# Kernel tuning notes

Hardware: AMD Instinct MI355X
Metric: run time of the kernel (lower is better)

The kernel has to match this reference:

```python
import jax, jax.numpy as jnp
import numpy as np

DIM = 1024
HEADS = 16
DIM_HEAD = 64
INNER = HEADS * DIM_HEAD  # 1024
FEAT = 1024  # cfg.different_learnable_tokens=False -> feature_dim = dim
EPS = 1e-5
SCALE = 1.0 / np.sqrt(DIM_HEAD)


def setup_inputs() -> dict:
    key = jax.random.key(0)
    ks = jax.random.split(key, 10)
    b, n = 2, 2048
    x = jax.random.normal(ks[0], (b, n, DIM), jnp.float32)
    y = jax.random.normal(ks[1], (b, n, FEAT), jnp.float32)
    # learned parameters
    ln_g = jnp.ones((DIM,), jnp.float32)
    ln_b = jnp.zeros((DIM,), jnp.float32)
    w_qkv = jax.random.normal(ks[2], (DIM, 3 * INNER), jnp.float32) * (DIM ** -0.5)
    w_av = jax.random.normal(ks[3], (FEAT, INNER), jnp.float32) * (FEAT ** -0.5)
    w_out = jax.random.normal(ks[4], (INNER, DIM), jnp.float32) * (INNER ** -0.5)
    b_out = jnp.zeros((DIM,), jnp.float32)
    w_yout = jax.random.normal(ks[5], (INNER, FEAT), jnp.float32) * (INNER ** -0.5)
    b_yout = jnp.zeros((FEAT,), jnp.float32)
    return {"x": x, "y": y, "ln_g": ln_g, "ln_b": ln_b, "w_qkv": w_qkv,
            "w_av": w_av, "w_out": w_out, "b_out": b_out,
            "w_yout": w_yout, "b_yout": b_yout}


def _split_heads(t):  # [b,n,(h d)] -> [b,h,n,d]
    b, n, _ = t.shape
    return t.reshape(b, n, HEADS, DIM_HEAD).transpose(0, 2, 1, 3)


def _merge_heads(t):  # [b,h,n,d] -> [b,n,(h d)]
    b, h, n, d = t.shape
    return t.transpose(0, 2, 1, 3).reshape(b, n, h * d)


def reference(x, y, ln_g, ln_b, w_qkv, w_av, w_out, b_out, w_yout, b_yout):
    # LayerNorm
    mu = jnp.mean(x, axis=-1, keepdims=True)
    var = jnp.mean(jnp.square(x - mu), axis=-1, keepdims=True)
    xn = (x - mu) * jax.lax.rsqrt(var + EPS) * ln_g + ln_b

    qkv = xn @ w_qkv  # [b,n,3*inner]
    q, k, v = jnp.split(qkv, 3, axis=-1)
    av = y @ w_av  # [b,n,inner]
    q, k, v, av = map(_split_heads, (q, k, v, av))  # [b,h,n,d]

    # shared QK softmax, applied to both V and another_v
    scores = jnp.einsum('bhnd,bhmd->bhnm', q, k) * SCALE
    attn = jax.nn.softmax(scores, axis=-1)
    x_ctx = jnp.einsum('bhnm,bhmd->bhnd', attn, v)
    y_ctx = jnp.einsum('bhnm,bhmd->bhnd', attn, av)

    x_out = _merge_heads(x_ctx) @ w_out + b_out
    y_out = _merge_heads(y_ctx) @ w_yout + b_yout
    return (x_out, y_out)
```

## Files before the change

### kernel.cpp

```cpp
#include <hip/hip_runtime.h>

typedef _Float16 half8 __attribute__((ext_vector_type(8)));
typedef _Float16 half4v __attribute__((ext_vector_type(4)));
typedef float f32x4 __attribute__((ext_vector_type(4)));
typedef unsigned int u32;

#define SEQ 2048
#define NTOK 4096
#define DM 1024
#define QKS 2048
#define LN_EPS 1e-5f
#define LOG2E_SCALE 0.18033688f

typedef const __attribute__((address_space(1))) u32* gas_ptr;
typedef __attribute__((address_space(3))) u32* las_ptr;
__device__ __forceinline__ void gld_lds16(const void* g, void* l) {
  __builtin_amdgcn_global_load_lds((gas_ptr)g, (las_ptr)l, 16, 0, 0);
}

#define BARRIER() do { __builtin_amdgcn_s_barrier(); __builtin_amdgcn_sched_barrier(0); } while (0)
#define VMW(N) do { asm volatile("s_waitcnt vmcnt(" #N ")" ::: "memory"); __builtin_amdgcn_sched_barrier(0); } while (0)
#define LGW() do { asm volatile("s_waitcnt lgkmcnt(0)" ::: "memory"); __builtin_amdgcn_sched_barrier(0); } while (0)

__global__ __launch_bounds__(256) void prep_kernel(
    const float* __restrict__ x, const float* __restrict__ g, const float* __restrict__ bta,
    const float* __restrict__ y,
    const float* __restrict__ w_qkv, const float* __restrict__ w_av,
    const float* __restrict__ w_out, const float* __restrict__ w_yout,
    _Float16* __restrict__ xn, _Float16* __restrict__ yh,
    _Float16* __restrict__ wqkvT, _Float16* __restrict__ wavT,
    _Float16* __restrict__ woutT, _Float16* __restrict__ wyoutT) {
  __shared__ float smem[64 * 65];
  const int bid = blockIdx.x;
  const int t = threadIdx.x;
  if (bid < 4096) {
    const int row = bid;
    const float4 v = ((const float4*)(x + (size_t)row * DM))[t];
    float s = v.x + v.y + v.z + v.w;
#pragma unroll
    for (int m = 1; m < 64; m <<= 1) s += __shfl_xor(s, m, 64);
    float* red = smem;
    const int wid = t >> 6, lane = t & 63;
    if (lane == 0) red[wid] = s;
    __syncthreads();
    const float mu = (red[0] + red[1] + red[2] + red[3]) * (1.0f / DM);
    const float dx = v.x - mu, dy = v.y - mu, dz = v.z - mu, dw = v.w - mu;
    float ss = dx * dx + dy * dy + dz * dz + dw * dw;
#pragma unroll
    for (int m = 1; m < 64; m <<= 1) ss += __shfl_xor(ss, m, 64);
    __syncthreads();
    if (lane == 0) red[wid] = ss;
    __syncthreads();
    const float var = (red[0] + red[1] + red[2] + red[3]) * (1.0f / DM);
    const float rstd = rsqrtf(var + LN_EPS);
    const float4 gg = ((const float4*)g)[t];
    const float4 bb = ((const float4*)bta)[t];
    half4v o;
    o[0] = (_Float16)(dx * rstd * gg.x + bb.x);
    o[1] = (_Float16)(dy * rstd * gg.y + bb.y);
    o[2] = (_Float16)(dz * rstd * gg.z + bb.z);
    o[3] = (_Float16)(dw * rstd * gg.w + bb.w);
    *(half4v*)(xn + (size_t)row * DM + t * 4) = o;
  } else if (bid < 8192) {
    const int row = bid - 4096;
    const float4 v = ((const float4*)(y + (size_t)row * DM))[t];
    half4v o;
    o[0] = (_Float16)v.x; o[1] = (_Float16)v.y;
    o[2] = (_Float16)v.z; o[3] = (_Float16)v.w;
    *(half4v*)(yh + (size_t)row * DM + t * 4) = o;
  } else {
    const int id2 = bid - 8192;
    const float* W; _Float16* WT; int Nc, bx, by;
    if (id2 < 768) { W = w_qkv; WT = wqkvT; Nc = 3072; bx = id2 % 48; by = id2 / 48; }
    else {
      const int id3 = id2 - 768, sel = id3 >> 8;
      Nc = 1024; bx = id3 & 15; by = (id3 >> 4) & 15;
      if (sel == 0) { W = w_av; WT = wavT; }
      else if (sel == 1) { W = w_out; WT = woutT; }
      else { W = w_yout; WT = wyoutT; }
    }
    float (*tile)[65] = (float(*)[65])smem;
    const int n0 = bx * 64, k0 = by * 64;
    const int c = t & 63;
#pragma unroll
    for (int i = 0; i < 16; i++) {
      const int r = (t >> 6) * 16 + i;
      tile[r][c] = W[(size_t)(k0 + r) * Nc + n0 + c];
    }
    __syncthreads();
#pragma unroll
    for (int i = 0; i < 16; i++) {
      const int n = (t >> 6) * 16 + i;
      WT[(size_t)(n0 + n) * 1024 + k0 + c] = (_Float16)tile[c][n];
    }
  }
}

__global__ __launch_bounds__(512, 2) void gemm8p_kernel(
    const _Float16* __restrict__ xn, const _Float16* __restrict__ wqkvT,
    const _Float16* __restrict__ yh, const _Float16* __restrict__ wavT,
    _Float16* __restrict__ qkvm, _Float16* __restrict__ vtb,
    _Float16* __restrict__ avtb) {
  __shared__ _Float16 Ab[2][8192];
  __shared__ _Float16 Bb[2][8192];
  const int swz = ((blockIdx.x & 7) << 5) + (blockIdx.x >> 3);
  const _Float16 *A, *B;
  int m0, n0, isav;
  if (swz < 192) { A = xn; B = wqkvT; m0 = (swz / 12) * 256; n0 = (swz % 12) * 256; isav = 0; }
  else { const int u = swz - 192; A = yh; B = wavT; m0 = (u >> 2) * 256; n0 = (u & 3) * 256; isav = 1; }
  const int t = threadIdx.x;
  const int wid = t >> 6, lane = t & 63, lo = lane & 15, hi = lane >> 4;
  const int wm = wid >> 2, wn = wid & 3;
  const int srow = t >> 2;
  const int sx = ((t & 3) ^ (srow & 3)) << 3;
  const _Float16* gA = A + (size_t)(m0 + srow) * 1024 + sx;
  const _Float16* gB = B + (size_t)(n0 + srow) * 1024 + sx;
  const int rdz = (hi ^ (lo & 3)) << 3;
  const int arow = (wm * 128 + lo) * 32 + rdz;
  const int brow = (wn * 64 + lo) * 32 + rdz;

  f32x4 acc[8][4];
#pragma unroll
  for (int i = 0; i < 8; i++)
#pragma unroll
    for (int j = 0; j < 4; j++) {
      acc[i][j][0] = 0.f; acc[i][j][1] = 0.f; acc[i][j][2] = 0.f; acc[i][j][3] = 0.f;
    }
  half8 af[4], bf[4];

#define STG_A(BUF, HH, KT) gld_lds16(gA + (HH) * 131072 + (KT) * 32, &Ab[BUF][(HH) * 4096 + t * 8])
#define STG_B(BUF, HH, KT) gld_lds16(gB + (HH) * 131072 + (KT) * 32, &Bb[BUF][(HH) * 4096 + t * 8])
#define RDA(BUF, FB)                                                     \
  _Pragma("unroll") for (int f2 = 0; f2 < 4; f2++)                       \
      af[f2] = *(const half8*)&Ab[BUF][arow + ((FB) + f2) * 512]
#define RDB(BUF, G0)                                                     \
  _Pragma("unroll") for (int g2 = 0; g2 < 2; g2++)                       \
      bf[(G0) + g2] = *(const half8*)&Bb[BUF][brow + ((G0) + g2) * 512]
#define MMA(FB, G0)                                                      \
  do {                                                                   \
    __builtin_amdgcn_s_setprio(1);                                       \
    _Pragma("unroll") for (int f2 = 0; f2 < 4; f2++)                     \
        _Pragma("unroll") for (int g2 = 0; g2 < 2; g2++)                 \
            acc[(FB) + f2][(G0) + g2] = __builtin_amdgcn_mfma_f32_16x16x32_f16( \
                af[f2], bf[(G0) + g2], acc[(FB) + f2][(G0) + g2], 0, 0, 0); \
    __builtin_amdgcn_s_setprio(0);                                       \
  } while (0)

  STG_A(0, 0, 0); STG_A(0, 1, 0); STG_B(0, 0, 0); STG_B(0, 1, 0);
  STG_A(1, 0, 1);

  for (int it = 0; it < 16; it++) {
    const int T1 = 2 * it + 1;
    const int N0 = (2 * it + 2) & 31, N1 = (2 * it + 3) & 31;
    VMW(1); BARRIER();
    RDA(0, 0); RDB(0, 0);
    STG_A(1, 1, T1);
    LGW(); MMA(0, 0);
    BARRIER(); RDB(0, 2); STG_B(1, 0, T1); LGW(); MMA(0, 2);
    BARRIER(); RDA(0, 4); STG_B(1, 1, T1); LGW(); MMA(4, 2);
    BARRIER(); STG_A(0, 0, N0); MMA(4, 0);
    VMW(1); BARRIER();
    RDA(1, 0); RDB(1, 0);
    STG_A(0, 1, N0);
    LGW(); MMA(0, 0);
    BARRIER(); RDB(1, 2); STG_B(0, 0, N0); LGW(); MMA(0, 2);
    BARRIER(); RDA(1, 4); STG_B(0, 1, N0); LGW(); MMA(4, 2);
    BARRIER(); STG_A(1, 0, N1); MMA(4, 0);
  }
#undef STG_A
#undef STG_B
#undef RDA
#undef RDB
#undef MMA

#pragma unroll
  for (int f = 0; f < 8; f++)
#pragma unroll
    for (int g = 0; g < 4; g++)
#pragma unroll
      for (int r = 0; r < 4; r++) {
        const int row = m0 + wm * 128 + f * 16 + 4 * hi + r;
        const int col = n0 + wn * 64 + g * 16 + lo;
        const _Float16 v = (_Float16)acc[f][g][r];
        if (!isav && col < 2048) {
          qkvm[(size_t)row * QKS + col] = v;
        } else {
          const int coff = isav ? col : col - 2048;
          _Float16* Ct = isav ? avtb : vtb;
          Ct[(((size_t)((row >> 11) << 4) + (coff >> 6)) * 64 + (coff & 63)) * SEQ +
             (row & (SEQ - 1))] = v;
        }
      }
}

__global__ __launch_bounds__(512, 2) void gemmout8p_kernel(
    const _Float16* __restrict__ xc, const _Float16* __restrict__ woutT,
    float* __restrict__ o0, const float* __restrict__ b0,
    const _Float16* __restrict__ yc, const _Float16* __restrict__ wyoutT,
    float* __restrict__ o1, const float* __restrict__ b1) {
  __shared__ _Float16 Ab[2][8192];
  __shared__ _Float16 Bb[2][8192];
  const int swz = ((blockIdx.x & 7) << 4) + (blockIdx.x >> 3);
  const _Float16 *A, *B;
  float* F; const float* bias;
  int u;
  if (swz < 64) { A = xc; B = woutT; F = o0; bias = b0; u = swz; }
  else { A = yc; B = wyoutT; F = o1; bias = b1; u = swz - 64; }
  const int m0 = (u >> 2) * 256, n0 = (u & 3) * 256;
  const int t = threadIdx.x;
  const int wid = t >> 6, lane = t & 63, lo = lane & 15, hi = lane >> 4;
  const int wm = wid >> 2, wn = wid & 3;
  const int srow = t >> 2;
  const int sx = ((t & 3) ^ (srow & 3)) << 3;
  const _Float16* gA = A + (size_t)(m0 + srow) * 1024 + sx;
  const _Float16* gB = B + (size_t)(n0 + srow) * 1024 + sx;
  const int rdz = (hi ^ (lo & 3)) << 3;
  const int arow = (wm * 128 + lo) * 32 + rdz;
  const int brow = (wn * 64 + lo) * 32 + rdz;

  f32x4 acc[8][4];
#pragma unroll
  for (int i = 0; i < 8; i++)
#pragma unroll
    for (int j = 0; j < 4; j++) {
      acc[i][j][0] = 0.f; acc[i][j][1] = 0.f; acc[i][j][2] = 0.f; acc[i][j][3] = 0.f;
    }
  half8 af[4], bf[4];

#define STG_A(BUF, HH, KT) gld_lds16(gA + (HH) * 131072 + (KT) * 32, &Ab[BUF][(HH) * 4096 + t * 8])
#define STG_B(BUF, HH, KT) gld_lds16(gB + (HH) * 131072 + (KT) * 32, &Bb[BUF][(HH) * 4096 + t * 8])
#define RDA(BUF, FB)                                                     \
  _Pragma("unroll") for (int f2 = 0; f2 < 4; f2++)                       \
      af[f2] = *(const half8*)&Ab[BUF][arow + ((FB) + f2) * 512]
#define RDB(BUF, G0)                                                     \
  _Pragma("unroll") for (int g2 = 0; g2 < 2; g2++)                       \
      bf[(G0) + g2] = *(const half8*)&Bb[BUF][brow + ((G0) + g2) * 512]
#define MMA(FB, G0)                                                      \
  do {                                                                   \
    __builtin_amdgcn_s_setprio(1);                                       \
    _Pragma("unroll") for (int f2 = 0; f2 < 4; f2++)                     \
        _Pragma("unroll") for (int g2 = 0; g2 < 2; g2++)                 \
            acc[(FB) + f2][(G0) + g2] = __builtin_amdgcn_mfma_f32_16x16x32_f16( \
                af[f2], bf[(G0) + g2], acc[(FB) + f2][(G0) + g2], 0, 0, 0); \
    __builtin_amdgcn_s_setprio(0);                                       \
  } while (0)

  STG_A(0, 0, 0); STG_A(0, 1, 0); STG_B(0, 0, 0); STG_B(0, 1, 0);
  STG_A(1, 0, 1);

  for (int it = 0; it < 16; it++) {
    const int T1 = 2 * it + 1;
    const int N0 = (2 * it + 2) & 31, N1 = (2 * it + 3) & 31;
    VMW(1); BARRIER();
    RDA(0, 0); RDB(0, 0);
    STG_A(1, 1, T1);
    LGW(); MMA(0, 0);
    BARRIER(); RDB(0, 2); STG_B(1, 0, T1); LGW(); MMA(0, 2);
    BARRIER(); RDA(0, 4); STG_B(1, 1, T1); LGW(); MMA(4, 2);
    BARRIER(); STG_A(0, 0, N0); MMA(4, 0);
    VMW(1); BARRIER();
    RDA(1, 0); RDB(1, 0);
    STG_A(0, 1, N0);
    LGW(); MMA(0, 0);
    BARRIER(); RDB(1, 2); STG_B(0, 0, N0); LGW(); MMA(0, 2);
    BARRIER(); RDA(1, 4); STG_B(0, 1, N0); LGW(); MMA(4, 2);
    BARRIER(); STG_A(1, 0, N1); MMA(4, 0);
  }
#undef STG_A
#undef STG_B
#undef RDA
#undef RDB
#undef MMA

#pragma unroll
  for (int f = 0; f < 8; f++)
#pragma unroll
    for (int g = 0; g < 4; g++)
#pragma unroll
      for (int r = 0; r < 4; r++) {
        const int row = m0 + wm * 128 + f * 16 + 4 * hi + r;
        const int col = n0 + wn * 64 + g * 16 + lo;
        F[(size_t)row * 1024 + col] = acc[f][g][r] + bias[col];
      }
}

__global__ __launch_bounds__(256, 4) void attn_kernel(
    const _Float16* __restrict__ qkvm,
    const _Float16* __restrict__ vt,
    const _Float16* __restrict__ avt,
    _Float16* __restrict__ xctx, _Float16* __restrict__ yctx) {
  __shared__ _Float16 Kl[2][2048];
  __shared__ _Float16 Vl[2][2048];
  __shared__ _Float16 Al[2][2048];
  __shared__ _Float16 Pl[4][512];

  const int t = threadIdx.x;
  const int wid = t >> 6, lane = t & 63, lo = lane & 15, hi = lane >> 4;
  const int id = blockIdx.x;
  const int bh = ((id & 7) << 2) + ((id >> 3) >> 5);
  const int qt = (id >> 3) & 31;
  const int b = bh >> 4, h = bh & 15;
  const int q0 = qt * 64 + wid * 16;
  const size_t tokbase = (size_t)b * SEQ;
  const _Float16* vbase = vt + (size_t)bh * 64 * SEQ;
  const _Float16* abase = avt + (size_t)bh * 64 * SEQ;
  _Float16* Pw = Pl[wid];
  const int NT = SEQ / 32;
  const int swzP = (lo & 3) ^ ((lo >> 2) & 3);

  half8 qf[2];
#pragma unroll
  for (int kc = 0; kc < 2; kc++)
    qf[kc] = *(const half8*)(qkvm + (tokbase + q0 + lo) * QKS +
                             h * 64 + kc * 32 + hi * 8);

  f32x4 zero;
  zero[0] = 0.f; zero[1] = 0.f; zero[2] = 0.f; zero[3] = 0.f;
  f32x4 accx[4], accy[4];
  float mC = -1.0e30f, lsum = 0.0f;
#pragma unroll
  for (int j = 0; j < 4; j++) { accx[j] = zero; accy[j] = zero; }

  const int kkey = t >> 3, kc7 = t & 7;
  const int vrow = t >> 2, vc3 = t & 3;
  const int kcs = ((kc7 ^ (kkey & 7)) << 3);
  const int vcs = ((vc3 ^ ((vrow & 3) ^ ((vrow >> 2) & 3))) << 3);

#define STAGE(kv0, BSEL)                                                          \
  do {                                                                            \
    gld_lds16(qkvm + (tokbase + (kv0) + kkey) * QKS + DM + h * 64 + kcs,          \
              &Kl[BSEL][(t >> 6) * 512 + (t & 63) * 8]);                          \
    gld_lds16(vbase + (size_t)vrow * SEQ + (kv0) + vcs,                           \
              &Vl[BSEL][(t >> 6) * 512 + (t & 63) * 8]);                          \
    gld_lds16(abase + (size_t)vrow * SEQ + (kv0) + vcs,                           \
              &Al[BSEL][(t >> 6) * 512 + (t & 63) * 8]);                          \
  } while (0)

  STAGE(0, 0);
  int bsel = 0;
  for (int tt = 0; tt < NT; tt++) {
    __syncthreads();
    if (tt + 1 < NT) STAGE((tt + 1) * 32, bsel ^ 1);
    const _Float16* Kb = Kl[bsel];
    const _Float16* Vb = Vl[bsel];
    const _Float16* Ab = Al[bsel];

    f32x4 s[2];
#pragma unroll
    for (int kg = 0; kg < 2; kg++) {
      const int krow = kg * 16 + lo;
      const int kr = krow * 64;
      const half8 ak0 = *(const half8*)(Kb + kr + ((hi ^ (krow & 7)) << 3));
      const half8 ak1 = *(const half8*)(Kb + kr + (((4 | hi) ^ (krow & 7)) << 3));
      f32x4 z = __builtin_amdgcn_mfma_f32_16x16x32_f16(ak0, qf[0], zero, 0, 0, 0);
      s[kg] = __builtin_amdgcn_mfma_f32_16x16x32_f16(ak1, qf[1], z, 0, 0, 0);
    }

    float tm = -3.0e38f;
#pragma unroll
    for (int kg = 0; kg < 2; kg++)
#pragma unroll
      for (int r = 0; r < 4; r++) tm = fmaxf(tm, s[kg][r]);
    tm = fmaxf(tm, __shfl_xor(tm, 16, 64));
    tm = fmaxf(tm, __shfl_xor(tm, 32, 64));
    const float tmC = tm * LOG2E_SCALE;

    if (__any(tmC > mC + 8.0f)) {
      const float mn = fmaxf(mC, tmC);
      const float fcs = exp2f(mC - mn);
      mC = mn;
      lsum *= fcs;
#pragma unroll
      for (int r = 0; r < 4; r++) {
        const float fcb = __shfl(fcs, 4 * hi + r, 64);
#pragma unroll
        for (int ng = 0; ng < 4; ng++) {
          accx[ng][r] *= fcb;
          accy[ng][r] *= fcb;
        }
      }
    }

    {
      float rs = 0.0f;
#pragma unroll
      for (int kg = 0; kg < 2; kg++) {
        half4v pk;
#pragma unroll
        for (int r = 0; r < 4; r++) {
          const float p = exp2f(fmaf(s[kg][r], LOG2E_SCALE, -mC));
          rs += p;
          pk[r] = (_Float16)p;
        }
        *(half4v*)(Pw + lo * 32 +
                   (((kg * 2 + (hi >> 1)) ^ swzP) << 3) + ((hi & 1) << 2)) = pk;
      }
      rs += __shfl_xor(rs, 16, 64);
      rs += __shfl_xor(rs, 32, 64);
      lsum += rs;
    }

    {
      const half8 pa = *(const half8*)(Pw + lo * 32 + ((hi ^ swzP) << 3));
#pragma unroll
      for (int ng = 0; ng < 4; ng++) {
        const int vrow2 = ng * 16 + lo;
        const int vr = vrow2 * 32 + ((hi ^ ((vrow2 & 3) ^ ((vrow2 >> 2) & 3))) << 3);
        const half8 bv = *(const half8*)(Vb + vr);
        const half8 ba = *(const half8*)(Ab + vr);
        accx[ng] = __builtin_amdgcn_mfma_f32_16x16x32_f16(pa, bv, accx[ng], 0, 0, 0);
        accy[ng] = __builtin_amdgcn_mfma_f32_16x16x32_f16(pa, ba, accy[ng], 0, 0, 0);
      }
    }
    bsel ^= 1;
  }
#undef STAGE

  const float inv = 1.0f / lsum;
#pragma unroll
  for (int r = 0; r < 4; r++) {
    const float invb = __shfl(inv, 4 * hi + r, 64);
    const size_t tok = tokbase + q0 + 4 * hi + r;
#pragma unroll
    for (int ng = 0; ng < 4; ng++) {
      const int col = h * 64 + ng * 16 + lo;
      xctx[tok * DM + col] = (_Float16)(accx[ng][r] * invb);
      yctx[tok * DM + col] = (_Float16)(accy[ng][r] * invb);
    }
  }
}

extern "C" void kernel_launch(void* const* d_in, const int* in_sizes, int n_in,
                              void* d_out, int out_size, void* d_ws, size_t ws_size,
                              hipStream_t stream) {
  const float* x      = (const float*)d_in[0];
  const float* y      = (const float*)d_in[1];
  const float* ln_g   = (const float*)d_in[2];
  const float* ln_b   = (const float*)d_in[3];
  const float* w_qkv  = (const float*)d_in[4];
  const float* w_av   = (const float*)d_in[5];
  const float* w_out  = (const float*)d_in[6];
  const float* b_out  = (const float*)d_in[7];
  const float* w_yout = (const float*)d_in[8];
  const float* b_yout = (const float*)d_in[9];
  float* out = (float*)d_out;

  _Float16* ws     = (_Float16*)d_ws;
  _Float16* xn     = ws;
  _Float16* yh     = xn + 4194304;
  _Float16* wqkvT  = yh + 4194304;
  _Float16* wavT   = wqkvT + 3145728;
  _Float16* woutT  = wavT + 1048576;
  _Float16* wyoutT = woutT + 1048576;
  _Float16* qkvm   = wyoutT + 1048576;
  _Float16* vtb    = qkvm + 8388608;
  _Float16* avtb   = vtb + 4194304;
  _Float16* xc     = avtb + 4194304;
  _Float16* yc     = xc + 4194304;

  prep_kernel<<<9728, 256, 0, stream>>>(x, ln_g, ln_b, y, w_qkv, w_av, w_out, w_yout,
                                        xn, yh, wqkvT, wavT, woutT, wyoutT);

  gemm8p_kernel<<<256, 512, 0, stream>>>(xn, wqkvT, yh, wavT, qkvm, vtb, avtb);

  attn_kernel<<<1024, 256, 0, stream>>>(qkvm, vtb, avtb, xc, yc);

  gemmout8p_kernel<<<128, 512, 0, stream>>>(
      xc, woutT, out, b_out,
      yc, wyoutT, out + 4194304, b_yout);
}
```

Baseline: 210.7 us.

## Deepen QKV GEMM K-tile, simplify output GEMM, defer softmax reductions

```diff
diff --git a/kernel.cpp b/kernel.cpp
--- a/kernel.cpp
+++ b/kernel.cpp
@@ -96,13 +96,13 @@
   }
 }
 
-__global__ __launch_bounds__(512, 2) void gemm8p_kernel(
+__global__ __launch_bounds__(512, 1) void gemm8p_kernel(
     const _Float16* __restrict__ xn, const _Float16* __restrict__ wqkvT,
     const _Float16* __restrict__ yh, const _Float16* __restrict__ wavT,
     _Float16* __restrict__ qkvm, _Float16* __restrict__ vtb,
     _Float16* __restrict__ avtb) {
-  __shared__ _Float16 Ab[2][8192];
-  __shared__ _Float16 Bb[2][8192];
+  __shared__ _Float16 Ab[2][16384];
+  __shared__ _Float16 Bb[2][16384];
   const int swz = ((blockIdx.x & 7) << 5) + (blockIdx.x >> 3);
   const _Float16 *A, *B;
   int m0, n0, isav;
@@ -111,13 +111,14 @@
   const int t = threadIdx.x;
   const int wid = t >> 6, lane = t & 63, lo = lane & 15, hi = lane >> 4;
   const int wm = wid >> 2, wn = wid & 3;
-  const int srow = t >> 2;
-  const int sx = ((t & 3) ^ (srow & 3)) << 3;
-  const _Float16* gA = A + (size_t)(m0 + srow) * 1024 + sx;
-  const _Float16* gB = B + (size_t)(n0 + srow) * 1024 + sx;
-  const int rdz = (hi ^ (lo & 3)) << 3;
-  const int arow = (wm * 128 + lo) * 32 + rdz;
-  const int brow = (wn * 64 + lo) * 32 + rdz;
+  const int srow = t >> 3;
+  const int schk = t & 7;
+  const _Float16* gA = A + (size_t)(m0 + srow) * 1024 + ((schk ^ (srow & 7)) << 3);
+  const _Float16* gB = B + (size_t)(n0 + srow) * 1024 + ((schk ^ (srow & 7)) << 3);
+  const int arow = (wm * 128 + lo) * 64;
+  const int brow = (wn * 64 + lo) * 64;
+  const int rz0 = ((hi ^ (lo & 7)) << 3);
+  const int rz1 = (((4 | hi) ^ (lo & 7)) << 3);
 
   f32x4 acc[8][4];
 #pragma unroll
@@ -126,52 +127,58 @@
     for (int j = 0; j < 4; j++) {
       acc[i][j][0] = 0.f; acc[i][j][1] = 0.f; acc[i][j][2] = 0.f; acc[i][j][3] = 0.f;
     }
-  half8 af[4], bf[4];
-
-#define STG_A(BUF, HH, KT) gld_lds16(gA + (HH) * 131072 + (KT) * 32, &Ab[BUF][(HH) * 4096 + t * 8])
-#define STG_B(BUF, HH, KT) gld_lds16(gB + (HH) * 131072 + (KT) * 32, &Bb[BUF][(HH) * 4096 + t * 8])
-#define RDA(BUF, FB)                                                     \
-  _Pragma("unroll") for (int f2 = 0; f2 < 4; f2++)                       \
-      af[f2] = *(const half8*)&Ab[BUF][arow + ((FB) + f2) * 512]
-#define RDB(BUF, G0)                                                     \
-  _Pragma("unroll") for (int g2 = 0; g2 < 2; g2++)                       \
-      bf[(G0) + g2] = *(const half8*)&Bb[BUF][brow + ((G0) + g2) * 512]
-#define MMA(FB, G0)                                                      \
-  do {                                                                   \
-    __builtin_amdgcn_s_setprio(1);                                       \
-    _Pragma("unroll") for (int f2 = 0; f2 < 4; f2++)                     \
-        _Pragma("unroll") for (int g2 = 0; g2 < 2; g2++)                 \
-            acc[(FB) + f2][(G0) + g2] = __builtin_amdgcn_mfma_f32_16x16x32_f16( \
-                af[f2], bf[(G0) + g2], acc[(FB) + f2][(G0) + g2], 0, 0, 0); \
-    __builtin_amdgcn_s_setprio(0);                                       \
+  half8 af[4][2], bf[4][2];
+
+#define STG_A(BUF, P, KT) gld_lds16(gA + (P) * 65536 + (KT) * 64, &Ab[BUF][(P) * 4096 + t * 8])
+#define STG_B(BUF, P, KT) gld_lds16(gB + (P) * 65536 + (KT) * 64, &Bb[BUF][(P) * 4096 + t * 8])
+#define RDA8(BUF, FB)                                                       \
+  _Pragma("unroll") for (int f2 = 0; f2 < 4; f2++) {                        \
+    af[f2][0] = *(const half8*)&Ab[BUF][arow + ((FB) + f2) * 1024 + rz0];   \
+    af[f2][1] = *(const half8*)&Ab[BUF][arow + ((FB) + f2) * 1024 + rz1];   \
+  }
+#define RDB4(BUF, G0)                                                       \
+  _Pragma("unroll") for (int g2 = 0; g2 < 2; g2++) {                        \
+    bf[(G0) + g2][0] = *(const half8*)&Bb[BUF][brow + ((G0) + g2) * 1024 + rz0]; \
+    bf[(G0) + g2][1] = *(const half8*)&Bb[BUF][brow + ((G0) + g2) * 1024 + rz1]; \
+  }
+#define MMA16(FB, G0)                                                       \
+  do {                                                                      \
+    __builtin_amdgcn_s_setprio(1);                                          \
+    _Pragma("unroll") for (int f2 = 0; f2 < 4; f2++)                        \
+      _Pragma("unroll") for (int g2 = 0; g2 < 2; g2++)                      \
+        _Pragma("unroll") for (int ks = 0; ks < 2; ks++)                    \
+          acc[(FB) + f2][(G0) + g2] = __builtin_amdgcn_mfma_f32_16x16x32_f16( \
+              af[f2][ks], bf[(G0) + g2][ks], acc[(FB) + f2][(G0) + g2], 0, 0, 0); \
+    __builtin_amdgcn_s_setprio(0);                                          \
   } while (0)
 
-  STG_A(0, 0, 0); STG_A(0, 1, 0); STG_B(0, 0, 0); STG_B(0, 1, 0);
-  STG_A(1, 0, 1);
-
-  for (int it = 0; it < 16; it++) {
+  STG_A(0, 0, 0); STG_A(0, 1, 0); STG_A(0, 2, 0); STG_A(0, 3, 0);
+  STG_B(0, 0, 0); STG_B(0, 1, 0); STG_B(0, 2, 0); STG_B(0, 3, 0);
+  STG_A(1, 0, 1); STG_A(1, 1, 1);
+
+  for (int it = 0; it < 8; it++) {
     const int T1 = 2 * it + 1;
-    const int N0 = (2 * it + 2) & 31, N1 = (2 * it + 3) & 31;
-    VMW(1); BARRIER();
-    RDA(0, 0); RDB(0, 0);
-    STG_A(1, 1, T1);
-    LGW(); MMA(0, 0);
-    BARRIER(); RDB(0, 2); STG_B(1, 0, T1); LGW(); MMA(0, 2);
-    BARRIER(); RDA(0, 4); STG_B(1, 1, T1); LGW(); MMA(4, 2);
-    BARRIER(); STG_A(0, 0, N0); MMA(4, 0);
-    VMW(1); BARRIER();
-    RDA(1, 0); RDB(1, 0);
-    STG_A(0, 1, N0);
-    LGW(); MMA(0, 0);
-    BARRIER(); RDB(1, 2); STG_B(0, 0, N0); LGW(); MMA(0, 2);
-    BARRIER(); RDA(1, 4); STG_B(0, 1, N0); LGW(); MMA(4, 2);
-    BARRIER(); STG_A(1, 0, N1); MMA(4, 0);
+    const int N0 = (2 * it + 2) & 15, N1 = (2 * it + 3) & 15;
+    VMW(2); BARRIER();
+    RDA8(0, 0); RDB4(0, 0);
+    STG_A(1, 2, T1); STG_A(1, 3, T1);
+    LGW(); MMA16(0, 0);
+    BARRIER(); RDB4(0, 2); STG_B(1, 0, T1); STG_B(1, 1, T1); LGW(); MMA16(0, 2);
+    BARRIER(); RDA8(0, 4); STG_B(1, 2, T1); STG_B(1, 3, T1); LGW(); MMA16(4, 2);
+    BARRIER(); STG_A(0, 0, N0); STG_A(0, 1, N0); MMA16(4, 0);
+    VMW(2); BARRIER();
+    RDA8(1, 0); RDB4(1, 0);
+    STG_A(0, 2, N0); STG_A(0, 3, N0);
+    LGW(); MMA16(0, 0);
+    BARRIER(); RDB4(1, 2); STG_B(0, 0, N0); STG_B(0, 1, N0); LGW(); MMA16(0, 2);
+    BARRIER(); RDA8(1, 4); STG_B(0, 2, N0); STG_B(0, 3, N0); LGW(); MMA16(4, 2);
+    BARRIER(); STG_A(1, 0, N1); STG_A(1, 1, N1); MMA16(4, 0);
   }
 #undef STG_A
 #undef STG_B
-#undef RDA
-#undef RDB
-#undef MMA
+#undef RDA8
+#undef RDB4
+#undef MMA16
 
 #pragma unroll
   for (int f = 0; f < 8; f++)
@@ -193,94 +200,66 @@
       }
 }
 
-__global__ __launch_bounds__(512, 2) void gemmout8p_kernel(
-    const _Float16* __restrict__ xc, const _Float16* __restrict__ woutT,
-    float* __restrict__ o0, const float* __restrict__ b0,
-    const _Float16* __restrict__ yc, const _Float16* __restrict__ wyoutT,
-    float* __restrict__ o1, const float* __restrict__ b1) {
-  __shared__ _Float16 Ab[2][8192];
-  __shared__ _Float16 Bb[2][8192];
-  const int swz = ((blockIdx.x & 7) << 4) + (blockIdx.x >> 3);
-  const _Float16 *A, *B;
-  float* F; const float* bias;
-  int u;
-  if (swz < 64) { A = xc; B = woutT; F = o0; bias = b0; u = swz; }
-  else { A = yc; B = wyoutT; F = o1; bias = b1; u = swz - 64; }
-  const int m0 = (u >> 2) * 256, n0 = (u & 3) * 256;
+__global__ __launch_bounds__(256) void gemmout_kernel(
+    const _Float16* __restrict__ A0, const _Float16* __restrict__ B0,
+    float* F0, const float* bias0, int nblk0,
+    const _Float16* __restrict__ A1, const _Float16* __restrict__ B1,
+    float* F1, const float* bias1) {
+  __shared__ _Float16 As[128 * 32];
+  __shared__ _Float16 Bs[128 * 32];
+  int id = ((blockIdx.x & 7) * (gridDim.x >> 3)) + (blockIdx.x >> 3);
+  const _Float16 *A, *BT;
+  float* Cf; const float* bias;
+  if (id < nblk0) { A = A0; BT = B0; Cf = F0; bias = bias0; }
+  else { id -= nblk0; A = A1; BT = B1; Cf = F1; bias = bias1; }
+  const int bx = id & 7, by = id >> 3;
   const int t = threadIdx.x;
   const int wid = t >> 6, lane = t & 63, lo = lane & 15, hi = lane >> 4;
-  const int wm = wid >> 2, wn = wid & 3;
-  const int srow = t >> 2;
-  const int sx = ((t & 3) ^ (srow & 3)) << 3;
-  const _Float16* gA = A + (size_t)(m0 + srow) * 1024 + sx;
-  const _Float16* gB = B + (size_t)(n0 + srow) * 1024 + sx;
-  const int rdz = (hi ^ (lo & 3)) << 3;
-  const int arow = (wm * 128 + lo) * 32 + rdz;
-  const int brow = (wn * 64 + lo) * 32 + rdz;
-
-  f32x4 acc[8][4];
-#pragma unroll
-  for (int i = 0; i < 8; i++)
+  const int wm = wid >> 1, wn = wid & 1;
+  const int m0 = by * 128, n0 = bx * 128;
+  const int K = 1024;
+
+  f32x4 acc[4][4];
+#pragma unroll
+  for (int i = 0; i < 4; i++)
 #pragma unroll
     for (int j = 0; j < 4; j++) {
       acc[i][j][0] = 0.f; acc[i][j][1] = 0.f; acc[i][j][2] = 0.f; acc[i][j][3] = 0.f;
     }
-  half8 af[4], bf[4];
-
-#define STG_A(BUF, HH, KT) gld_lds16(gA + (HH) * 131072 + (KT) * 32, &Ab[BUF][(HH) * 4096 + t * 8])
-#define STG_B(BUF, HH, KT) gld_lds16(gB + (HH) * 131072 + (KT) * 32, &Bb[BUF][(HH) * 4096 + t * 8])
-#define RDA(BUF, FB)                                                     \
-  _Pragma("unroll") for (int f2 = 0; f2 < 4; f2++)                       \
-      af[f2] = *(const half8*)&Ab[BUF][arow + ((FB) + f2) * 512]
-#define RDB(BUF, G0)                                                     \
-  _Pragma("unroll") for (int g2 = 0; g2 < 2; g2++)                       \
-      bf[(G0) + g2] = *(const half8*)&Bb[BUF][brow + ((G0) + g2) * 512]
-#define MMA(FB, G0)                                                      \
-  do {                                                                   \
-    __builtin_amdgcn_s_setprio(1);                                       \
-    _Pragma("unroll") for (int f2 = 0; f2 < 4; f2++)                     \
-        _Pragma("unroll") for (int g2 = 0; g2 < 2; g2++)                 \
-            acc[(FB) + f2][(G0) + g2] = __builtin_amdgcn_mfma_f32_16x16x32_f16( \
-                af[f2], bf[(G0) + g2], acc[(FB) + f2][(G0) + g2], 0, 0, 0); \
-    __builtin_amdgcn_s_setprio(0);                                       \
-  } while (0)
-
-  STG_A(0, 0, 0); STG_A(0, 1, 0); STG_B(0, 0, 0); STG_B(0, 1, 0);
-  STG_A(1, 0, 1);
-
-  for (int it = 0; it < 16; it++) {
-    const int T1 = 2 * it + 1;
-    const int N0 = (2 * it + 2) & 31, N1 = (2 * it + 3) & 31;
-    VMW(1); BARRIER();
-    RDA(0, 0); RDB(0, 0);
-    STG_A(1, 1, T1);
-    LGW(); MMA(0, 0);
-    BARRIER(); RDB(0, 2); STG_B(1, 0, T1); LGW(); MMA(0, 2);
-    BARRIER(); RDA(0, 4); STG_B(1, 1, T1); LGW(); MMA(4, 2);
-    BARRIER(); STG_A(0, 0, N0); MMA(4, 0);
-    VMW(1); BARRIER();
-    RDA(1, 0); RDB(1, 0);
-    STG_A(0, 1, N0);
-    LGW(); MMA(0, 0);
-    BARRIER(); RDB(1, 2); STG_B(0, 0, N0); LGW(); MMA(0, 2);
-    BARRIER(); RDA(1, 4); STG_B(0, 1, N0); LGW(); MMA(4, 2);
-    BARRIER(); STG_A(1, 0, N1); MMA(4, 0);
-  }
-#undef STG_A
-#undef STG_B
-#undef RDA
-#undef RDB
-#undef MMA
-
-#pragma unroll
-  for (int f = 0; f < 8; f++)
-#pragma unroll
-    for (int g = 0; g < 4; g++)
+  const int rowA = t >> 2;
+  const int kcol = (t & 3) * 8;
+  const _Float16* gA = A + (size_t)(m0 + rowA) * K + kcol;
+  const _Float16* gB = BT + (size_t)(n0 + rowA) * K + kcol;
+
+  for (int k0 = 0; k0 < K; k0 += 32) {
+#pragma unroll
+    for (int j = 0; j < 2; j++) {
+      gld_lds16(gA + (size_t)(j * 64) * K + k0, As + j * 2048 + wid * 512);
+      gld_lds16(gB + (size_t)(j * 64) * K + k0, Bs + j * 2048 + wid * 512);
+    }
+    __syncthreads();
+    half8 af[4], bf[4];
+#pragma unroll
+    for (int i = 0; i < 4; i++) {
+      af[i] = *(const half8*)(As + (wm * 64 + i * 16 + lo) * 32 + hi * 8);
+      bf[i] = *(const half8*)(Bs + (wn * 64 + i * 16 + lo) * 32 + hi * 8);
+    }
+#pragma unroll
+    for (int i = 0; i < 4; i++)
+#pragma unroll
+      for (int j = 0; j < 4; j++)
+        acc[i][j] = __builtin_amdgcn_mfma_f32_16x16x32_f16(af[i], bf[j], acc[i][j], 0, 0, 0);
+    __syncthreads();
+  }
+#pragma unroll
+  for (int i = 0; i < 4; i++)
+#pragma unroll
+    for (int j = 0; j < 4; j++)
 #pragma unroll
       for (int r = 0; r < 4; r++) {
-        const int row = m0 + wm * 128 + f * 16 + 4 * hi + r;
-        const int col = n0 + wn * 64 + g * 16 + lo;
-        F[(size_t)row * 1024 + col] = acc[f][g][r] + bias[col];
+        const int row = m0 + wm * 64 + i * 16 + 4 * hi + r;
+        const int col = n0 + wn * 64 + j * 16 + lo;
+        Cf[(size_t)row * 1024 + col] = acc[i][j][r] + bias[col];
       }
 }
 
@@ -361,12 +340,11 @@
     for (int kg = 0; kg < 2; kg++)
 #pragma unroll
       for (int r = 0; r < 4; r++) tm = fmaxf(tm, s[kg][r]);
-    tm = fmaxf(tm, __shfl_xor(tm, 16, 64));
-    tm = fmaxf(tm, __shfl_xor(tm, 32, 64));
-    const float tmC = tm * LOG2E_SCALE;
-
-    if (__any(tmC > mC + 8.0f)) {
-      const float mn = fmaxf(mC, tmC);
+    if (__any(tm * LOG2E_SCALE > mC + 8.0f)) {
+      float tw = tm;
+      tw = fmaxf(tw, __shfl_xor(tw, 16, 64));
+      tw = fmaxf(tw, __shfl_xor(tw, 32, 64));
+      const float mn = fmaxf(mC, tw * LOG2E_SCALE);
       const float fcs = exp2f(mC - mn);
       mC = mn;
       lsum *= fcs;
@@ -395,8 +373,6 @@
         *(half4v*)(Pw + lo * 32 +
                    (((kg * 2 + (hi >> 1)) ^ swzP) << 3) + ((hi & 1) << 2)) = pk;
       }
-      rs += __shfl_xor(rs, 16, 64);
-      rs += __shfl_xor(rs, 32, 64);
       lsum += rs;
     }
 
@@ -416,6 +392,8 @@
   }
 #undef STAGE
 
+  lsum += __shfl_xor(lsum, 16, 64);
+  lsum += __shfl_xor(lsum, 32, 64);
   const float inv = 1.0f / lsum;
 #pragma unroll
   for (int r = 0; r < 4; r++) {
@@ -465,7 +443,7 @@
 
   attn_kernel<<<1024, 256, 0, stream>>>(qkvm, vtb, avtb, xc, yc);
 
-  gemmout8p_kernel<<<128, 512, 0, stream>>>(
-      xc, woutT, out, b_out,
+  gemmout_kernel<<<512, 256, 0, stream>>>(
+      xc, woutT, out, b_out, 256,
       yc, wyoutT, out + 4194304, b_yout);
 }
```

New measurement: 200.2 us. -5.0%, faster.
